# Optimization experiments

Measured on AMD Instinct MI355X. Metric: run time of the kernel, lower is better.

## Reference

```python
import jax, jax.numpy as jnp
import numpy as np

B, T, C = 2, 2048, 1024
N_HEAD = 16
HEAD = C // N_HEAD  # 64


def setup_inputs() -> dict:
    key = jax.random.key(0)
    k1, k2, k3, k4, k5 = jax.random.split(key, 5)
    s = 1.0 / np.sqrt(C)
    return {
        "x": jax.random.normal(k1, (B, T, C), dtype=jnp.float32),
        "w_qkv": jax.random.normal(k2, (C, 3 * C), dtype=jnp.float32) * s,
        "b_qkv": jax.random.normal(k3, (3 * C,), dtype=jnp.float32) * 0.01,
        "w_proj": jax.random.normal(k4, (C, C), dtype=jnp.float32) * s,
        "b_proj": jax.random.normal(k5, (C,), dtype=jnp.float32) * 0.01,
    }


def reference(x, w_qkv, b_qkv, w_proj, b_proj):
    b, t, c = x.shape
    # QKV projection -> (3, B, H, T, head)
    qkv = (x @ w_qkv + b_qkv).reshape(b, t, 3, N_HEAD, HEAD).transpose(2, 0, 3, 1, 4)
    q, k, v = qkv[0], qkv[1], qkv[2]
    # scaled causal attention scores [B,H,T,T]
    att = jnp.einsum("bhqd,bhkd->bhqk", q, k) * (HEAD ** -0.5)
    causal = jnp.tril(jnp.ones((t, t), dtype=bool))
    att = jnp.where(causal, att, jnp.float32(-jnp.inf))
    att = jax.nn.softmax(att, axis=-1)
    out = jnp.einsum("bhqk,bhkd->bhqd", att, v)  # [B,H,T,head]
    out = out.transpose(0, 2, 1, 3).reshape(b, t, c)
    # dropout is identity in eval mode (p effectively 0)
    return out @ w_proj + b_proj
```

## Files before the change

kernel.cpp:

```cpp
#include <hip/hip_runtime.h>
#include <cstdint>

typedef __attribute__((ext_vector_type(8))) short bf16x8_t;
typedef __attribute__((ext_vector_type(4))) float f32x4_t;
typedef __attribute__((ext_vector_type(16))) float f32x16_t;

#define T_SEQ 2048
#define NHEAD 16
#define CDIM  1024

__device__ __forceinline__ unsigned short f2bf(float f) {
  union { float f; unsigned u; } v; v.f = f;
  unsigned r = v.u + 0x7FFFu + ((v.u >> 16) & 1u);
  return (unsigned short)(r >> 16);
}

__device__ __forceinline__ float fast_exp2(float x) {
#if __has_builtin(__builtin_amdgcn_exp2f)
  return __builtin_amdgcn_exp2f(x);
#else
  return __expf(x * 0.6931471805599453f);
#endif
}

__device__ __forceinline__ unsigned cvtpk(float lo, float hi) {
  unsigned r;
  asm("v_cvt_pk_bf16_f32 %0, %1, %2" : "=v"(r) : "v"(lo), "v"(hi));
  return r;
}
#define PLSWAP(a, b) asm("v_permlane32_swap_b32 %0, %1" : "+v"(a), "+v"(b))

__device__ __forceinline__ void gload_lds16(const void* g, void* l) {
  typedef const uint32_t __attribute__((address_space(1)))* gp_t;
  typedef uint32_t __attribute__((address_space(3)))* lp_t;
  __builtin_amdgcn_global_load_lds((gp_t)(uintptr_t)g, (lp_t)(uint32_t)(uintptr_t)l, 16, 0, 0);
}

__global__ void conv_bf16_kernel(const float* __restrict__ in,
                                 unsigned short* __restrict__ out, int n4) {
  int i = blockIdx.x * blockDim.x + threadIdx.x;
  if (i >= n4) return;
  float4 v = ((const float4*)in)[i];
  ushort4 o;
  o.x = f2bf(v.x); o.y = f2bf(v.y); o.z = f2bf(v.z); o.w = f2bf(v.w);
  ((ushort4*)out)[i] = o;
}

__global__ void transpose_bf16_kernel(const float* __restrict__ W,
                                      unsigned short* __restrict__ WT, int R, int C) {
  __shared__ unsigned short tile[64][65];
  const int c0 = blockIdx.x * 64, r0 = blockIdx.y * 64;
  const int t = threadIdx.x;
  #pragma unroll
  for (int i = 0; i < 16; i++) {
    int idx = i * 256 + t;
    int r = idx >> 6, c = idx & 63;
    tile[r][c] = f2bf(W[(size_t)(r0 + r) * C + c0 + c]);
  }
  __syncthreads();
  #pragma unroll
  for (int i = 0; i < 16; i++) {
    int idx = i * 256 + t;
    int c = idx >> 6, r = idx & 63;
    WT[(size_t)(c0 + c) * R + r0 + r] = tile[r][c];
  }
}

template <int MODE>
__global__ void gemm_bt_kernel(const unsigned short* __restrict__ A,
                               const unsigned short* __restrict__ Bt,
                               const float* __restrict__ bias,
                               unsigned short* __restrict__ q_out,
                               unsigned short* __restrict__ k_out,
                               unsigned short* __restrict__ v_out,
                               float* __restrict__ c_out) {
  constexpr int K = 1024;
  constexpr int TN = (MODE == 0) ? 128 : 64;
  constexpr int NF = TN / 32;
  const int t = threadIdx.x;
  const int w = t >> 6, l = t & 63;
  const int lr = l & 15, lg = l >> 4;
  const int wr = w >> 1, wc = w & 1;
  const int m0 = blockIdx.y * 128, n0 = blockIdx.x * TN;

  __shared__ __align__(16) unsigned short As[128 * 64];
  __shared__ __align__(16) unsigned short Bs[TN * 64];

  f32x4_t acc[4][NF];
  #pragma unroll
  for (int mi = 0; mi < 4; mi++)
    #pragma unroll
    for (int ni = 0; ni < NF; ni++)
      acc[mi][ni] = (f32x4_t){0.f, 0.f, 0.f, 0.f};

  const int srow = t >> 3;
  const int sj   = t & 7;
  const int scol = (sj ^ (srow & 7)) * 8;
  const int ldst = srow * 64 + sj * 8;
  const size_t abase = (size_t)(m0 + srow) * K + scol;
  const size_t bbase = (size_t)(n0 + srow) * K + scol;

  for (int k0 = 0; k0 < K; k0 += 64) {
    __syncthreads();
    #pragma unroll
    for (int i = 0; i < 4; i++)
      gload_lds16(A + abase + (size_t)i * 32 * K + k0, &As[i * 32 * 64 + ldst]);
    #pragma unroll
    for (int i = 0; i < TN / 32; i++)
      gload_lds16(Bt + bbase + (size_t)i * 32 * K + k0, &Bs[i * 32 * 64 + ldst]);
    __syncthreads();
    #pragma unroll
    for (int ks = 0; ks < 2; ks++) {
      bf16x8_t af[4], bfr[NF];
      #pragma unroll
      for (int mi = 0; mi < 4; mi++) {
        const int row = wr * 64 + mi * 16 + lr;
        af[mi] = *(const bf16x8_t*)&As[row * 64 + (((ks * 4 + lg) ^ (row & 7)) << 3)];
      }
      #pragma unroll
      for (int ni = 0; ni < NF; ni++) {
        const int row = wc * (TN / 2) + ni * 16 + lr;
        bfr[ni] = *(const bf16x8_t*)&Bs[row * 64 + (((ks * 4 + lg) ^ (row & 7)) << 3)];
      }
      #pragma unroll
      for (int mi = 0; mi < 4; mi++)
        #pragma unroll
        for (int ni = 0; ni < NF; ni++)
          acc[mi][ni] = __builtin_amdgcn_mfma_f32_16x16x32_bf16(af[mi], bfr[ni], acc[mi][ni], 0, 0, 0);
    }
  }

  if (MODE == 0) {
    const float QSCALE = 0.125f * 1.4426950408889634f;
    #pragma unroll
    for (int ni = 0; ni < NF; ni++) {
      const int n = n0 + wc * 64 + ni * 16 + lr;
      const float bv = bias[n];
      const int s = n >> 10;
      const int hh = (n >> 6) & 15;
      const int d = n & 63;
      #pragma unroll
      for (int mi = 0; mi < 4; mi++) {
        const int mbase = m0 + wr * 64 + mi * 16 + lg * 4;
        const int batch = mbase >> 11;
        const int tt = mbase & 2047;
        const int bhh = batch * NHEAD + hh;
        if (s == 0) {
          #pragma unroll
          for (int r = 0; r < 4; r++)
            q_out[((size_t)bhh * T_SEQ + tt + r) * 64 + d] = f2bf((acc[mi][ni][r] + bv) * QSCALE);
        } else if (s == 1) {
          #pragma unroll
          for (int r = 0; r < 4; r++) {
            const int dsw = ((((d >> 3) ^ ((tt + r) & 7)) << 3) | (d & 7));
            k_out[((size_t)bhh * T_SEQ + tt + r) * 64 + dsw] = f2bf(acc[mi][ni][r] + bv);
          }
        } else {
          ushort4 pk;
          pk.x = f2bf(acc[mi][ni][0] + bv);
          pk.y = f2bf(acc[mi][ni][1] + bv);
          pk.z = f2bf(acc[mi][ni][2] + bv);
          pk.w = f2bf(acc[mi][ni][3] + bv);
          const int c2 = (((tt >> 3) & 7) ^ (d & 7));
          const int tt2 = (tt & ~63) | (c2 << 3) | (tt & 7);
          *(ushort4*)&v_out[((size_t)bhh * 64 + d) * T_SEQ + tt2] = pk;
        }
      }
    }
  } else {
    #pragma unroll
    for (int ni = 0; ni < NF; ni++) {
      const int n = n0 + wc * 32 + ni * 16 + lr;
      const float bv = bias[n];
      #pragma unroll
      for (int mi = 0; mi < 4; mi++) {
        const int m = m0 + wr * 64 + mi * 16 + lg * 4;
        #pragma unroll
        for (int r = 0; r < 4; r++)
          c_out[(size_t)(m + r) * 1024 + n] = acc[mi][ni][r] + bv;
      }
    }
  }
}

__global__ __launch_bounds__(256, 2)
void attn_kernel(const unsigned short* __restrict__ Qb,
                 const unsigned short* __restrict__ Kswz,
                 const unsigned short* __restrict__ Vswz,
                 unsigned short* __restrict__ O) {
  const int b0 = blockIdx.x;
  const int xcd = b0 & 7;
  const int i = b0 >> 3;
  const int bh = xcd * 4 + (i & 3);
  const int strip = 15 - (i >> 2);
  const int batch = bh >> 4, h = bh & 15;
  const int q0 = strip * 128;
  const int nT = 2 * strip + 2;

  const int t = threadIdx.x;
  const int w = t >> 6, l = t & 63;
  const int q31 = l & 31, hi = l >> 5;

  __shared__ __align__(16) unsigned short Ks[2][64 * 64];
  __shared__ __align__(16) unsigned short Vs[2][64 * 64];

  const size_t kvbase = (size_t)bh * T_SEQ;

  auto stage = [&](int buf, int kv0) {
    #pragma unroll
    for (int i2 = 0; i2 < 2; i2++) {
      const int r0 = w * 16 + i2 * 8;
      gload_lds16(Kswz + (kvbase + kv0 + r0 + (l >> 3)) * 64 + (l & 7) * 8,
                  &Ks[buf][r0 * 64 + l * 8]);
      gload_lds16(Vswz + ((size_t)bh * 64 + r0 + (l >> 3)) * T_SEQ + kv0 + (l & 7) * 8,
                  &Vs[buf][r0 * 64 + l * 8]);
    }
  };

  bf16x8_t qf[4];
  #pragma unroll
  for (int ds = 0; ds < 4; ds++)
    qf[ds] = *(const bf16x8_t*)&Qb[(kvbase + q0 + w * 32 + q31) * 64 + ds * 16 + hi * 8];

  f32x16_t accO[2];
  #pragma unroll
  for (int di = 0; di < 2; di++)
    #pragma unroll
    for (int j = 0; j < 16; j++) accO[di][j] = 0.f;
  float l_part = 0.f;

  stage(0, 0);
  __syncthreads();
  int cur = 0;

  for (int ti = 0; ti < nT; ++ti) {
    if (ti + 1 < nT) stage(cur ^ 1, (ti + 1) * 64);

    const bool active = !(ti == nT - 1 && w < 2);
    if (active) {
      f32x16_t sc[2];
      #pragma unroll
      for (int c = 0; c < 2; c++)
        #pragma unroll
        for (int j = 0; j < 16; j++) sc[c][j] = 0.f;
      #pragma unroll
      for (int ds = 0; ds < 4; ds++) {
        #pragma unroll
        for (int c = 0; c < 2; c++) {
          const int row = c * 32 + q31;
          bf16x8_t ka = *(const bf16x8_t*)&Ks[cur][row * 64 + (((ds * 2 + hi) ^ (row & 7)) << 3)];
          sc[c] = __builtin_amdgcn_mfma_f32_32x32x16_bf16(ka, qf[ds], sc[c], 0, 0, 0);
        }
      }

      if ((ti == nT - 2 && w < 2) || (ti == nT - 1 && w >= 2)) {
        const int lb = (ti == nT - 1) ? 64 : 0;
        const int ql = w * 32 + q31;
        #pragma unroll
        for (int c = 0; c < 2; c++)
          #pragma unroll
          for (int r = 0; r < 16; r++) {
            const int kvl = lb + c * 32 + (r & 3) + 8 * (r >> 2) + 4 * hi;
            if (kvl > ql) sc[c][r] = -1e30f;
          }
      }

      #pragma unroll
      for (int c = 0; c < 2; c++) {
        float p[16];
        #pragma unroll
        for (int r = 0; r < 16; r++) {
          p[r] = fast_exp2(sc[c][r]);
          l_part += p[r];
        }
        unsigned pk0 = cvtpk(p[0], p[1]),   pk1 = cvtpk(p[2], p[3]);
        unsigned pk2 = cvtpk(p[4], p[5]),   pk3 = cvtpk(p[6], p[7]);
        unsigned pk4 = cvtpk(p[8], p[9]),   pk5 = cvtpk(p[10], p[11]);
        unsigned pk6 = cvtpk(p[12], p[13]), pk7 = cvtpk(p[14], p[15]);

        PLSWAP(pk0, pk2);
        PLSWAP(pk1, pk3);
        union { unsigned u[4]; bf16x8_t v; } pb0 = {{pk0, pk1, pk2, pk3}};
        {
          const int s = c * 2;
          #pragma unroll
          for (int di = 0; di < 2; di++) {
            const int row = di * 32 + q31;
            bf16x8_t va = *(const bf16x8_t*)&Vs[cur][row * 64 + (((s * 2 + hi) ^ (row & 7)) << 3)];
            accO[di] = __builtin_amdgcn_mfma_f32_32x32x16_bf16(va, pb0.v, accO[di], 0, 0, 0);
          }
        }
        PLSWAP(pk4, pk6);
        PLSWAP(pk5, pk7);
        union { unsigned u[4]; bf16x8_t v; } pb1 = {{pk4, pk5, pk6, pk7}};
        {
          const int s = c * 2 + 1;
          #pragma unroll
          for (int di = 0; di < 2; di++) {
            const int row = di * 32 + q31;
            bf16x8_t va = *(const bf16x8_t*)&Vs[cur][row * 64 + (((s * 2 + hi) ^ (row & 7)) << 3)];
            accO[di] = __builtin_amdgcn_mfma_f32_32x32x16_bf16(va, pb1.v, accO[di], 0, 0, 0);
          }
        }
      }
    }

    __syncthreads();
    cur ^= 1;
  }

  const float l_tot = l_part + __shfl_xor(l_part, 32);
  const float rl = 1.0f / l_tot;
  const int q = q0 + w * 32 + q31;
  unsigned short* orow = O + ((size_t)batch * T_SEQ + q) * CDIM + h * 64;
  #pragma unroll
  for (int di = 0; di < 2; di++)
    #pragma unroll
    for (int g = 0; g < 4; g++) {
      const unsigned w0 = cvtpk(accO[di][4 * g] * rl, accO[di][4 * g + 1] * rl);
      const unsigned w1 = cvtpk(accO[di][4 * g + 2] * rl, accO[di][4 * g + 3] * rl);
      const int d = di * 32 + 8 * g + 4 * hi;
      uint2 pr; pr.x = w0; pr.y = w1;
      *(uint2*)&orow[d] = pr;
    }
}

extern "C" void kernel_launch(void* const* d_in, const int* in_sizes, int n_in,
                              void* d_out, int out_size, void* d_ws, size_t ws_size,
                              hipStream_t stream) {
  (void)in_sizes; (void)n_in; (void)out_size; (void)ws_size;
  const float* x      = (const float*)d_in[0];
  const float* w_qkv  = (const float*)d_in[1];
  const float* b_qkv  = (const float*)d_in[2];
  const float* w_proj = (const float*)d_in[3];
  const float* b_proj = (const float*)d_in[4];
  float* out = (float*)d_out;

  char* ws = (char*)d_ws;
  unsigned short* xb     = (unsigned short*)(ws);
  unsigned short* wqkvT  = (unsigned short*)(ws + ((size_t)8  << 20));
  unsigned short* wprojT = (unsigned short*)(ws + ((size_t)14 << 20));
  unsigned short* qb     = (unsigned short*)(ws + ((size_t)16 << 20));
  unsigned short* kb     = (unsigned short*)(ws + ((size_t)24 << 20));
  unsigned short* vtb    = (unsigned short*)(ws + ((size_t)32 << 20));
  unsigned short* ab     = (unsigned short*)(ws + ((size_t)40 << 20));

  conv_bf16_kernel<<<4096, 256, 0, stream>>>(x, xb, (2 * T_SEQ * CDIM) / 4);
  transpose_bf16_kernel<<<dim3(48, 16), 256, 0, stream>>>(w_qkv, wqkvT, 1024, 3072);
  transpose_bf16_kernel<<<dim3(16, 16), 256, 0, stream>>>(w_proj, wprojT, 1024, 1024);
  gemm_bt_kernel<0><<<dim3(24, 32), 256, 0, stream>>>(xb, wqkvT, b_qkv, qb, kb, vtb, nullptr);
  attn_kernel<<<512, 256, 0, stream>>>(qb, kb, vtb, ab);
  gemm_bt_kernel<1><<<dim3(16, 32), 256, 0, stream>>>(ab, wprojT, b_proj, nullptr, nullptr, nullptr, out);
}
```

Baseline: 102.3 us.

## Rewrite QKV GEMM as 256x256-tile 8-wave double-buffered pipelined kernel

Replaces the generic templated QKV GEMM with a dedicated kernel that uses 256x256 output tiles, 512 threads and double-buffered LDS. It interleaves asynchronous global-to-LDS loads with MFMA phases using explicit waitcnt, barriers and setprio. It also remaps block IDs so consecutive blocks spread across XCDs. The aim is to hide global-load latency and raise arithmetic intensity per tile, at the cost of much larger LDS use (128KB) and register pressure that limits occupancy to one block per CU. The projection GEMM is split into its own non-templated kernel with unchanged behaviour.

```diff
diff --git a/kernel.cpp b/kernel.cpp
--- a/kernel.cpp
+++ b/kernel.cpp
@@ -66,31 +66,180 @@
   }
 }
 
-template <int MODE>
-__global__ void gemm_bt_kernel(const unsigned short* __restrict__ A,
-                               const unsigned short* __restrict__ Bt,
-                               const float* __restrict__ bias,
-                               unsigned short* __restrict__ q_out,
-                               unsigned short* __restrict__ k_out,
-                               unsigned short* __restrict__ v_out,
-                               float* __restrict__ c_out) {
+__global__ __launch_bounds__(512)
+void gemm_qkv_8ph(const unsigned short* __restrict__ A,
+                  const unsigned short* __restrict__ Bt,
+                  const float* __restrict__ bias,
+                  unsigned short* __restrict__ q_out,
+                  unsigned short* __restrict__ k_out,
+                  unsigned short* __restrict__ v_out) {
   constexpr int K = 1024;
-  constexpr int TN = (MODE == 0) ? 128 : 64;
-  constexpr int NF = TN / 32;
+  const int t = threadIdx.x;
+  const int wid = t >> 6, l = t & 63;
+  const int wm = wid >> 2, wn = wid & 3;
+  const int lr = l & 15, lg = l >> 4;
+
+  const int b0 = blockIdx.x;
+  const int wg = (b0 & 7) * 24 + (b0 >> 3);
+  const int m0 = (wg / 12) * 256;
+  const int n0 = (wg % 12) * 256;
+
+  __shared__ __align__(16) unsigned short As[2][2][128 * 64];
+  __shared__ __align__(16) unsigned short Bs[2][2][128 * 64];
+
+  f32x4_t acc[8][4];
+  #pragma unroll
+  for (int mi = 0; mi < 8; mi++)
+    #pragma unroll
+    for (int ni = 0; ni < 4; ni++)
+      acc[mi][ni] = (f32x4_t){0.f, 0.f, 0.f, 0.f};
+
+  auto stgA = [&](int kt, int h) {
+    const int slot = kt & 1;
+    #pragma unroll
+    for (int j = 0; j < 2; j++) {
+      const int flat = j * 512 + t;
+      const int row = flat >> 3, ch = flat & 7;
+      gload_lds16(A + (size_t)(m0 + h * 128 + row) * K + kt * 64 + ((ch ^ (row & 7)) << 3),
+                  &As[slot][h][flat * 8]);
+    }
+  };
+  auto stgB = [&](int kt, int h) {
+    const int slot = kt & 1;
+    #pragma unroll
+    for (int j = 0; j < 2; j++) {
+      const int flat = j * 512 + t;
+      const int row = flat >> 3, ch = flat & 7;
+      gload_lds16(Bt + (size_t)(n0 + h * 128 + row) * K + kt * 64 + ((ch ^ (row & 7)) << 3),
+                  &Bs[slot][h][flat * 8]);
+    }
+  };
+
+  stgA(0, 0); stgA(0, 1); stgB(0, 0); stgB(0, 1);
+  stgB(1, 0); stgB(1, 1);
+  asm volatile("s_waitcnt vmcnt(4)" ::: "memory");
+  __builtin_amdgcn_s_barrier();
+
+  bf16x8_t bfrag[4][2];
+
+  for (int it = 0; it < 8; ++it) {
+    const bool more = (it < 7);
+    const int tb = 2 * it + 1;
+    #pragma unroll
+    for (int half = 0; half < 2; ++half) {
+      #pragma unroll
+      for (int p = 0; p < 4; ++p) {
+        bf16x8_t a[2][2];
+        #pragma unroll
+        for (int mm = 0; mm < 2; ++mm) {
+          const int row = (2 * p + mm) * 16 + lr;
+          #pragma unroll
+          for (int ks = 0; ks < 2; ++ks)
+            a[mm][ks] = *(const bf16x8_t*)&As[half][wm][row * 64 + (((ks * 4 + lg) ^ (lr & 7)) << 3)];
+        }
+        if (p == 0) {
+          #pragma unroll
+          for (int ni = 0; ni < 4; ++ni) {
+            const int row = (wn & 1) * 64 + ni * 16 + lr;
+            #pragma unroll
+            for (int ks = 0; ks < 2; ++ks)
+              bfrag[ni][ks] = *(const bf16x8_t*)&Bs[half][wn >> 1][row * 64 + (((ks * 4 + lg) ^ (lr & 7)) << 3)];
+          }
+        }
+        if (half == 0) {
+          if (p == 0)            { stgA(tb, 0); stgA(tb, 1); }
+          else if (p == 1 && more) stgB(tb + 1, 0);
+          else if (p == 2 && more) stgB(tb + 1, 1);
+        } else {
+          if (p == 0 && more)      stgA(tb + 1, 0);
+          else if (p == 1 && more) stgA(tb + 1, 1);
+          else if (p == 2 && more) stgB(tb + 2, 0);
+          else if (p == 3 && more) stgB(tb + 2, 1);
+        }
+        __builtin_amdgcn_s_barrier();
+        asm volatile("s_waitcnt lgkmcnt(0)" ::: "memory");
+        __builtin_amdgcn_sched_barrier(0);
+        __builtin_amdgcn_s_setprio(1);
+        #pragma unroll
+        for (int mm = 0; mm < 2; ++mm)
+          #pragma unroll
+          for (int ni = 0; ni < 4; ++ni)
+            #pragma unroll
+            for (int ks = 0; ks < 2; ++ks)
+              acc[2 * p + mm][ni] =
+                  __builtin_amdgcn_mfma_f32_16x16x32_bf16(a[mm][ks], bfrag[ni][ks],
+                                                          acc[2 * p + mm][ni], 0, 0, 0);
+        __builtin_amdgcn_s_setprio(0);
+        if (p == 3) {
+          if (half == 0) {
+            if (more) asm volatile("s_waitcnt vmcnt(4)" ::: "memory");
+            else      asm volatile("s_waitcnt vmcnt(0)" ::: "memory");
+          } else if (more) {
+            asm volatile("s_waitcnt vmcnt(4)" ::: "memory");
+          }
+        }
+        __builtin_amdgcn_s_barrier();
+      }
+    }
+  }
+
+  const float QSCALE = 0.125f * 1.4426950408889634f;
+  #pragma unroll
+  for (int ni = 0; ni < 4; ++ni) {
+    const int n = n0 + wn * 64 + ni * 16 + lr;
+    const float bv = bias[n];
+    const int s = n >> 10;
+    const int hh = (n >> 6) & 15;
+    const int d = n & 63;
+    #pragma unroll
+    for (int mi = 0; mi < 8; ++mi) {
+      const int mbase = m0 + wm * 128 + mi * 16 + lg * 4;
+      const int batch = mbase >> 11;
+      const int tt = mbase & 2047;
+      const int bhh = batch * NHEAD + hh;
+      if (s == 0) {
+        #pragma unroll
+        for (int r = 0; r < 4; r++)
+          q_out[((size_t)bhh * T_SEQ + tt + r) * 64 + d] = f2bf((acc[mi][ni][r] + bv) * QSCALE);
+      } else if (s == 1) {
+        #pragma unroll
+        for (int r = 0; r < 4; r++) {
+          const int dsw = ((((d >> 3) ^ ((tt + r) & 7)) << 3) | (d & 7));
+          k_out[((size_t)bhh * T_SEQ + tt + r) * 64 + dsw] = f2bf(acc[mi][ni][r] + bv);
+        }
+      } else {
+        ushort4 pk;
+        pk.x = f2bf(acc[mi][ni][0] + bv);
+        pk.y = f2bf(acc[mi][ni][1] + bv);
+        pk.z = f2bf(acc[mi][ni][2] + bv);
+        pk.w = f2bf(acc[mi][ni][3] + bv);
+        const int c2 = (((tt >> 3) & 7) ^ (d & 7));
+        const int tt2 = (tt & ~63) | (c2 << 3) | (tt & 7);
+        *(ushort4*)&v_out[((size_t)bhh * 64 + d) * T_SEQ + tt2] = pk;
+      }
+    }
+  }
+}
+
+__global__ void gemm_proj_kernel(const unsigned short* __restrict__ A,
+                                 const unsigned short* __restrict__ Bt,
+                                 const float* __restrict__ bias,
+                                 float* __restrict__ c_out) {
+  constexpr int K = 1024;
   const int t = threadIdx.x;
   const int w = t >> 6, l = t & 63;
   const int lr = l & 15, lg = l >> 4;
   const int wr = w >> 1, wc = w & 1;
-  const int m0 = blockIdx.y * 128, n0 = blockIdx.x * TN;
+  const int m0 = blockIdx.y * 128, n0 = blockIdx.x * 64;
 
   __shared__ __align__(16) unsigned short As[128 * 64];
-  __shared__ __align__(16) unsigned short Bs[TN * 64];
-
-  f32x4_t acc[4][NF];
+  __shared__ __align__(16) unsigned short Bs[64 * 64];
+
+  f32x4_t acc[4][2];
   #pragma unroll
   for (int mi = 0; mi < 4; mi++)
     #pragma unroll
-    for (int ni = 0; ni < NF; ni++)
+    for (int ni = 0; ni < 2; ni++)
       acc[mi][ni] = (f32x4_t){0.f, 0.f, 0.f, 0.f};
 
   const int srow = t >> 3;
@@ -106,79 +255,40 @@
     for (int i = 0; i < 4; i++)
       gload_lds16(A + abase + (size_t)i * 32 * K + k0, &As[i * 32 * 64 + ldst]);
     #pragma unroll
-    for (int i = 0; i < TN / 32; i++)
+    for (int i = 0; i < 2; i++)
       gload_lds16(Bt + bbase + (size_t)i * 32 * K + k0, &Bs[i * 32 * 64 + ldst]);
     __syncthreads();
     #pragma unroll
     for (int ks = 0; ks < 2; ks++) {
-      bf16x8_t af[4], bfr[NF];
+      bf16x8_t af[4], bfr[2];
       #pragma unroll
       for (int mi = 0; mi < 4; mi++) {
         const int row = wr * 64 + mi * 16 + lr;
         af[mi] = *(const bf16x8_t*)&As[row * 64 + (((ks * 4 + lg) ^ (row & 7)) << 3)];
       }
       #pragma unroll
-      for (int ni = 0; ni < NF; ni++) {
-        const int row = wc * (TN / 2) + ni * 16 + lr;
+      for (int ni = 0; ni < 2; ni++) {
+        const int row = wc * 32 + ni * 16 + lr;
         bfr[ni] = *(const bf16x8_t*)&Bs[row * 64 + (((ks * 4 + lg) ^ (row & 7)) << 3)];
       }
       #pragma unroll
       for (int mi = 0; mi < 4; mi++)
         #pragma unroll
-        for (int ni = 0; ni < NF; ni++)
+        for (int ni = 0; ni < 2; ni++)
           acc[mi][ni] = __builtin_amdgcn_mfma_f32_16x16x32_bf16(af[mi], bfr[ni], acc[mi][ni], 0, 0, 0);
     }
   }
 
-  if (MODE == 0) {
-    const float QSCALE = 0.125f * 1.4426950408889634f;
-    #pragma unroll
-    for (int ni = 0; ni < NF; ni++) {
-      const int n = n0 + wc * 64 + ni * 16 + lr;
-      const float bv = bias[n];
-      const int s = n >> 10;
-      const int hh = (n >> 6) & 15;
-      const int d = n & 63;
-      #pragma unroll
-      for (int mi = 0; mi < 4; mi++) {
-        const int mbase = m0 + wr * 64 + mi * 16 + lg * 4;
-        const int batch = mbase >> 11;
-        const int tt = mbase & 2047;
-        const int bhh = batch * NHEAD + hh;
-        if (s == 0) {
-          #pragma unroll
-          for (int r = 0; r < 4; r++)
-            q_out[((size_t)bhh * T_SEQ + tt + r) * 64 + d] = f2bf((acc[mi][ni][r] + bv) * QSCALE);
-        } else if (s == 1) {
-          #pragma unroll
-          for (int r = 0; r < 4; r++) {
-            const int dsw = ((((d >> 3) ^ ((tt + r) & 7)) << 3) | (d & 7));
-            k_out[((size_t)bhh * T_SEQ + tt + r) * 64 + dsw] = f2bf(acc[mi][ni][r] + bv);
-          }
-        } else {
-          ushort4 pk;
-          pk.x = f2bf(acc[mi][ni][0] + bv);
-          pk.y = f2bf(acc[mi][ni][1] + bv);
-          pk.z = f2bf(acc[mi][ni][2] + bv);
-          pk.w = f2bf(acc[mi][ni][3] + bv);
-          const int c2 = (((tt >> 3) & 7) ^ (d & 7));
-          const int tt2 = (tt & ~63) | (c2 << 3) | (tt & 7);
-          *(ushort4*)&v_out[((size_t)bhh * 64 + d) * T_SEQ + tt2] = pk;
-        }
-      }
-    }
-  } else {
-    #pragma unroll
-    for (int ni = 0; ni < NF; ni++) {
-      const int n = n0 + wc * 32 + ni * 16 + lr;
-      const float bv = bias[n];
-      #pragma unroll
-      for (int mi = 0; mi < 4; mi++) {
-        const int m = m0 + wr * 64 + mi * 16 + lg * 4;
-        #pragma unroll
-        for (int r = 0; r < 4; r++)
-          c_out[(size_t)(m + r) * 1024 + n] = acc[mi][ni][r] + bv;
-      }
+  #pragma unroll
+  for (int ni = 0; ni < 2; ni++) {
+    const int n = n0 + wc * 32 + ni * 16 + lr;
+    const float bv = bias[n];
+    #pragma unroll
+    for (int mi = 0; mi < 4; mi++) {
+      const int m = m0 + wr * 64 + mi * 16 + lg * 4;
+      #pragma unroll
+      for (int r = 0; r < 4; r++)
+        c_out[(size_t)(m + r) * 1024 + n] = acc[mi][ni][r] + bv;
     }
   }
 }
@@ -348,7 +458,7 @@
   conv_bf16_kernel<<<4096, 256, 0, stream>>>(x, xb, (2 * T_SEQ * CDIM) / 4);
   transpose_bf16_kernel<<<dim3(48, 16), 256, 0, stream>>>(w_qkv, wqkvT, 1024, 3072);
   transpose_bf16_kernel<<<dim3(16, 16), 256, 0, stream>>>(w_proj, wprojT, 1024, 1024);
-  gemm_bt_kernel<0><<<dim3(24, 32), 256, 0, stream>>>(xb, wqkvT, b_qkv, qb, kb, vtb, nullptr);
+  gemm_qkv_8ph<<<192, 512, 0, stream>>>(xb, wqkvT, b_qkv, qb, kb, vtb);
   attn_kernel<<<512, 256, 0, stream>>>(qb, kb, vtb, ab);
-  gemm_bt_kernel<1><<<dim3(16, 32), 256, 0, stream>>>(ab, wprojT, b_proj, nullptr, nullptr, nullptr, out);
-}
+  gemm_proj_kernel<<<dim3(16, 32), 256, 0, stream>>>(ab, wprojT, b_proj, out);
+}
```

Result: faster. 99.88 us (-2.4%).

## Use two waves per attention block, each handling 64 query rows

Applied to the files above, without the earlier changes.

The attention kernel now runs with 128 threads (2 waves) instead of 256, and each wave processes two 32-row query groups. Every K and V fragment read from LDS is reused for two MFMAs. This halves LDS read traffic per MFMA and amortizes the K/V staging across more work per wave. In exchange register pressure roughly doubles for the accumulators and scores, and there are fewer waves per block to hide latency. Causal masking is reworked so that wave 0 skips the last tile.

```diff
diff --git a/kernel.cpp b/kernel.cpp
--- a/kernel.cpp
+++ b/kernel.cpp
@@ -183,7 +183,7 @@
   }
 }
 
-__global__ __launch_bounds__(256, 2)
+__global__ __launch_bounds__(128, 2)
 void attn_kernel(const unsigned short* __restrict__ Qb,
                  const unsigned short* __restrict__ Kswz,
                  const unsigned short* __restrict__ Vswz,
@@ -208,26 +208,29 @@
 
   auto stage = [&](int buf, int kv0) {
     #pragma unroll
-    for (int i2 = 0; i2 < 2; i2++) {
-      const int r0 = w * 16 + i2 * 8;
-      gload_lds16(Kswz + (kvbase + kv0 + r0 + (l >> 3)) * 64 + (l & 7) * 8,
-                  &Ks[buf][r0 * 64 + l * 8]);
-      gload_lds16(Vswz + ((size_t)bh * 64 + r0 + (l >> 3)) * T_SEQ + kv0 + (l & 7) * 8,
-                  &Vs[buf][r0 * 64 + l * 8]);
+    for (int i2 = 0; i2 < 4; i2++) {
+      const int flat = i2 * 128 + t;
+      const int row = flat >> 3, ch = flat & 7;
+      gload_lds16(Kswz + (kvbase + kv0 + row) * 64 + ch * 8, &Ks[buf][flat * 8]);
+      gload_lds16(Vswz + ((size_t)bh * 64 + row) * T_SEQ + kv0 + ch * 8, &Vs[buf][flat * 8]);
     }
   };
 
-  bf16x8_t qf[4];
-  #pragma unroll
-  for (int ds = 0; ds < 4; ds++)
-    qf[ds] = *(const bf16x8_t*)&Qb[(kvbase + q0 + w * 32 + q31) * 64 + ds * 16 + hi * 8];
-
-  f32x16_t accO[2];
-  #pragma unroll
-  for (int di = 0; di < 2; di++)
-    #pragma unroll
-    for (int j = 0; j < 16; j++) accO[di][j] = 0.f;
-  float l_part = 0.f;
+  bf16x8_t qf[2][4];
+  #pragma unroll
+  for (int g = 0; g < 2; g++)
+    #pragma unroll
+    for (int ds = 0; ds < 4; ds++)
+      qf[g][ds] = *(const bf16x8_t*)&Qb[(kvbase + q0 + w * 64 + g * 32 + q31) * 64 + ds * 16 + hi * 8];
+
+  f32x16_t accO[2][2];
+  #pragma unroll
+  for (int g = 0; g < 2; g++)
+    #pragma unroll
+    for (int di = 0; di < 2; di++)
+      #pragma unroll
+      for (int j = 0; j < 16; j++) accO[g][di][j] = 0.f;
+  float l_part[2] = {0.f, 0.f};
 
   stage(0, 0);
   __syncthreads();
@@ -236,72 +239,70 @@
   for (int ti = 0; ti < nT; ++ti) {
     if (ti + 1 < nT) stage(cur ^ 1, (ti + 1) * 64);
 
-    const bool active = !(ti == nT - 1 && w < 2);
+    const bool active = !(ti == nT - 1 && w == 0);
     if (active) {
-      f32x16_t sc[2];
-      #pragma unroll
-      for (int c = 0; c < 2; c++)
-        #pragma unroll
-        for (int j = 0; j < 16; j++) sc[c][j] = 0.f;
-      #pragma unroll
-      for (int ds = 0; ds < 4; ds++) {
+      f32x16_t sc[2][2];
+      #pragma unroll
+      for (int g = 0; g < 2; g++)
+        #pragma unroll
+        for (int c = 0; c < 2; c++)
+          #pragma unroll
+          for (int j = 0; j < 16; j++) sc[g][c][j] = 0.f;
+      #pragma unroll
+      for (int ds = 0; ds < 4; ds++)
         #pragma unroll
         for (int c = 0; c < 2; c++) {
           const int row = c * 32 + q31;
           bf16x8_t ka = *(const bf16x8_t*)&Ks[cur][row * 64 + (((ds * 2 + hi) ^ (row & 7)) << 3)];
-          sc[c] = __builtin_amdgcn_mfma_f32_32x32x16_bf16(ka, qf[ds], sc[c], 0, 0, 0);
+          sc[0][c] = __builtin_amdgcn_mfma_f32_32x32x16_bf16(ka, qf[0][ds], sc[0][c], 0, 0, 0);
+          sc[1][c] = __builtin_amdgcn_mfma_f32_32x32x16_bf16(ka, qf[1][ds], sc[1][c], 0, 0, 0);
         }
-      }
-
-      if ((ti == nT - 2 && w < 2) || (ti == nT - 1 && w >= 2)) {
-        const int lb = (ti == nT - 1) ? 64 : 0;
-        const int ql = w * 32 + q31;
-        #pragma unroll
-        for (int c = 0; c < 2; c++)
+
+      if (ti == nT - 2 + w) {
+        #pragma unroll
+        for (int g = 0; g < 2; g++)
+          #pragma unroll
+          for (int c = 0; c < 2; c++)
+            #pragma unroll
+            for (int r = 0; r < 16; r++) {
+              const int kvl = c * 32 + (r & 3) + 8 * (r >> 2) + 4 * hi;
+              if (kvl > g * 32 + q31) sc[g][c][r] = -1e30f;
+            }
+      }
+
+      #pragma unroll
+      for (int c = 0; c < 2; c++) {
+        bf16x8_t pbA[2], pbB[2];
+        #pragma unroll
+        for (int g = 0; g < 2; g++) {
+          float p[16];
           #pragma unroll
           for (int r = 0; r < 16; r++) {
-            const int kvl = lb + c * 32 + (r & 3) + 8 * (r >> 2) + 4 * hi;
-            if (kvl > ql) sc[c][r] = -1e30f;
+            p[r] = fast_exp2(sc[g][c][r]);
+            l_part[g] += p[r];
           }
-      }
-
-      #pragma unroll
-      for (int c = 0; c < 2; c++) {
-        float p[16];
-        #pragma unroll
-        for (int r = 0; r < 16; r++) {
-          p[r] = fast_exp2(sc[c][r]);
-          l_part += p[r];
+          unsigned pk0 = cvtpk(p[0], p[1]),   pk1 = cvtpk(p[2], p[3]);
+          unsigned pk2 = cvtpk(p[4], p[5]),   pk3 = cvtpk(p[6], p[7]);
+          unsigned pk4 = cvtpk(p[8], p[9]),   pk5 = cvtpk(p[10], p[11]);
+          unsigned pk6 = cvtpk(p[12], p[13]), pk7 = cvtpk(p[14], p[15]);
+          PLSWAP(pk0, pk2); PLSWAP(pk1, pk3);
+          PLSWAP(pk4, pk6); PLSWAP(pk5, pk7);
+          union { unsigned u[4]; bf16x8_t v; } ua = {{pk0, pk1, pk2, pk3}};
+          union { unsigned u[4]; bf16x8_t v; } ub = {{pk4, pk5, pk6, pk7}};
+          pbA[g] = ua.v;
+          pbB[g] = ub.v;
         }
-        unsigned pk0 = cvtpk(p[0], p[1]),   pk1 = cvtpk(p[2], p[3]);
-        unsigned pk2 = cvtpk(p[4], p[5]),   pk3 = cvtpk(p[6], p[7]);
-        unsigned pk4 = cvtpk(p[8], p[9]),   pk5 = cvtpk(p[10], p[11]);
-        unsigned pk6 = cvtpk(p[12], p[13]), pk7 = cvtpk(p[14], p[15]);
-
-        PLSWAP(pk0, pk2);
-        PLSWAP(pk1, pk3);
-        union { unsigned u[4]; bf16x8_t v; } pb0 = {{pk0, pk1, pk2, pk3}};
-        {
-          const int s = c * 2;
+        #pragma unroll
+        for (int sl = 0; sl < 2; sl++) {
+          const int s = c * 2 + sl;
           #pragma unroll
           for (int di = 0; di < 2; di++) {
             const int row = di * 32 + q31;
             bf16x8_t va = *(const bf16x8_t*)&Vs[cur][row * 64 + (((s * 2 + hi) ^ (row & 7)) << 3)];
-            accO[di] = __builtin_amdgcn_mfma_f32_32x32x16_bf16(va, pb0.v, accO[di], 0, 0, 0);
+            accO[0][di] = __builtin_amdgcn_mfma_f32_32x32x16_bf16(va, sl ? pbB[0] : pbA[0], accO[0][di], 0, 0, 0);
+            accO[1][di] = __builtin_amdgcn_mfma_f32_32x32x16_bf16(va, sl ? pbB[1] : pbA[1], accO[1][di], 0, 0, 0);
           }
         }
-        PLSWAP(pk4, pk6);
-        PLSWAP(pk5, pk7);
-        union { unsigned u[4]; bf16x8_t v; } pb1 = {{pk4, pk5, pk6, pk7}};
-        {
-          const int s = c * 2 + 1;
-          #pragma unroll
-          for (int di = 0; di < 2; di++) {
-            const int row = di * 32 + q31;
-            bf16x8_t va = *(const bf16x8_t*)&Vs[cur][row * 64 + (((s * 2 + hi) ^ (row & 7)) << 3)];
-            accO[di] = __builtin_amdgcn_mfma_f32_32x32x16_bf16(va, pb1.v, accO[di], 0, 0, 0);
-          }
-        }
       }
     }
 
@@ -309,20 +310,23 @@
     cur ^= 1;
   }
 
-  const float l_tot = l_part + __shfl_xor(l_part, 32);
-  const float rl = 1.0f / l_tot;
-  const int q = q0 + w * 32 + q31;
-  unsigned short* orow = O + ((size_t)batch * T_SEQ + q) * CDIM + h * 64;
-  #pragma unroll
-  for (int di = 0; di < 2; di++)
-    #pragma unroll
-    for (int g = 0; g < 4; g++) {
-      const unsigned w0 = cvtpk(accO[di][4 * g] * rl, accO[di][4 * g + 1] * rl);
-      const unsigned w1 = cvtpk(accO[di][4 * g + 2] * rl, accO[di][4 * g + 3] * rl);
-      const int d = di * 32 + 8 * g + 4 * hi;
-      uint2 pr; pr.x = w0; pr.y = w1;
-      *(uint2*)&orow[d] = pr;
-    }
+  #pragma unroll
+  for (int g = 0; g < 2; g++) {
+    const float l_tot = l_part[g] + __shfl_xor(l_part[g], 32);
+    const float rl = 1.0f / l_tot;
+    const int q = q0 + w * 64 + g * 32 + q31;
+    unsigned short* orow = O + ((size_t)batch * T_SEQ + q) * CDIM + h * 64;
+    #pragma unroll
+    for (int di = 0; di < 2; di++)
+      #pragma unroll
+      for (int gg = 0; gg < 4; gg++) {
+        const unsigned w0 = cvtpk(accO[g][di][4 * gg] * rl, accO[g][di][4 * gg + 1] * rl);
+        const unsigned w1 = cvtpk(accO[g][di][4 * gg + 2] * rl, accO[g][di][4 * gg + 3] * rl);
+        const int d = di * 32 + 8 * gg + 4 * hi;
+        uint2 pr; pr.x = w0; pr.y = w1;
+        *(uint2*)&orow[d] = pr;
+      }
+  }
 }
 
 extern "C" void kernel_launch(void* const* d_in, const int* in_sizes, int n_in,
@@ -349,6 +353,6 @@
   transpose_bf16_kernel<<<dim3(48, 16), 256, 0, stream>>>(w_qkv, wqkvT, 1024, 3072);
   transpose_bf16_kernel<<<dim3(16, 16), 256, 0, stream>>>(w_proj, wprojT, 1024, 1024);
   gemm_bt_kernel<0><<<dim3(24, 32), 256, 0, stream>>>(xb, wqkvT, b_qkv, qb, kb, vtb, nullptr);
-  attn_kernel<<<512, 256, 0, stream>>>(qb, kb, vtb, ab);
+  attn_kernel<<<512, 128, 0, stream>>>(qb, kb, vtb, ab);
   gemm_bt_kernel<1><<<dim3(16, 32), 256, 0, stream>>>(ab, wprojT, b_proj, nullptr, nullptr, nullptr, out);
 }
```

New measurement: 115.3 us. 1.13x slower.
